# Performance work log

Measured on AMD Instinct MI355X. Metric: run time of the kernel, lower is better.

## Reference

```python
import jax, jax.numpy as jnp
import numpy as np

NEG = -1e9

def _lstm(x, Wih, Whh, b):
    # x: [B,S,D]; PyTorch gate order i,f,g,o; Wih:[4H,D], Whh:[4H,H], b:[4H]
    B = x.shape[0]
    H = Whh.shape[1]
    def step(carry, xt):
        h, c = carry
        g = xt @ Wih.T + h @ Whh.T + b
        i, f, gg, o = jnp.split(g, 4, axis=-1)
        c = jax.nn.sigmoid(f) * c + jax.nn.sigmoid(i) * jnp.tanh(gg)
        h = jax.nn.sigmoid(o) * jnp.tanh(c)
        return (h, c), h
    init = (jnp.zeros((B, H), x.dtype), jnp.zeros((B, H), x.dtype))
    _, hs = jax.lax.scan(step, init, x.transpose(1, 0, 2))
    return hs.transpose(1, 0, 2)  # [B,S,H]

def _bilstm(x, Wih_f, Whh_f, b_f, Wih_b, Whh_b, b_b):
    fwd = _lstm(x, Wih_f, Whh_f, b_f)
    bwd = jnp.flip(_lstm(jnp.flip(x, 1), Wih_b, Whh_b, b_b), 1)
    return jnp.concatenate([fwd, bwd], axis=-1)

def _windowed_attention(h, attn_W, attn_b, window_size):
    # score(i,j) = W @ [h_i, h_j, h_i*h_j] + b, decomposed exactly:
    #   = h_i@w1 + h_j@w2 + (h_i*w3)@h_j + b, masked to |i-j| <= window
    S = h.shape[1]
    w1, w2, w3 = jnp.split(attn_W[0], 3)
    s1 = h @ w1                                   # [B,S]
    s2 = h @ w2                                   # [B,S]
    cross = jnp.einsum('bid,bjd->bij', h * w3, h)  # [B,S,S]
    scores = s1[:, :, None] + s2[:, None, :] + cross + attn_b[0]
    idx = jnp.arange(S)
    band = jnp.abs(idx[:, None] - idx[None, :]) <= window_size
    scores = jnp.where(band, scores, NEG)
    p = jax.nn.softmax(scores, axis=-1)
    return jnp.einsum('bij,bjd->bid', p, h)       # [B,S,H]

def _forward(x, lstm1_Wih_f, lstm1_Whh_f, lstm1_b_f, lstm1_Wih_b, lstm1_Whh_b, lstm1_b_b,
             fc1_W, fc1_b, attn_W, attn_b,
             lstm2_Wih_f, lstm2_Whh_f, lstm2_b_f, lstm2_Wih_b, lstm2_Whh_b, lstm2_b_b,
             l2_W1, l2_b1, l2_W2, l2_b2, l2_W3, l2_b3, window_size):
    # dropout layers are identity at inference
    lstm_out = _bilstm(x, lstm1_Wih_f, lstm1_Whh_f, lstm1_b_f,
                       lstm1_Wih_b, lstm1_Whh_b, lstm1_b_b)          # [B,S,768]
    h = lstm_out @ fc1_W.T + fc1_b                                    # [B,S,384]
    attn = _windowed_attention(h, attn_W, attn_b, window_size)        # [B,S,384]
    h_cat = jnp.concatenate([h, attn], axis=-1)                       # [B,S,768]
    lstm_out2 = _bilstm(h_cat, lstm2_Wih_f, lstm2_Whh_f, lstm2_b_f,
                        lstm2_Wih_b, lstm2_Whh_b, lstm2_b_b)          # [B,S,768]
    h2 = lstm_out2 @ fc1_W.T + fc1_b                                  # fc1 reused, as in source
    y = jax.nn.relu(h2 @ l2_W1.T + l2_b1)
    y = jax.nn.relu(y @ l2_W2.T + l2_b2)
    return y @ l2_W3.T + l2_b3                                        # [B,S,1]

def setup_inputs() -> dict:
    key = jax.random.key(0)
    ks = iter(jax.random.split(key, 32))
    D, H, B, S = 768, 384, 16, 1024
    sc = 0.02
    def rn(shape):
        return jax.random.normal(next(ks), shape, dtype=jnp.float32) * sc
    inp = {'x': jax.random.normal(next(ks), (B, S, D), dtype=jnp.float32)}
    for name in ('lstm1', 'lstm2'):
        inp[f'{name}_Wih_f'] = rn((4 * H, D)); inp[f'{name}_Whh_f'] = rn((4 * H, H))
        inp[f'{name}_b_f'] = rn((4 * H,))
        inp[f'{name}_Wih_b'] = rn((4 * H, D)); inp[f'{name}_Whh_b'] = rn((4 * H, H))
        inp[f'{name}_b_b'] = rn((4 * H,))
    inp['fc1_W'] = rn((H, D)); inp['fc1_b'] = rn((H,))
    inp['attn_W'] = rn((1, 3 * H)); inp['attn_b'] = rn((1,))
    inp['l2_W1'] = rn((256, H)); inp['l2_b1'] = rn((256,))
    inp['l2_W2'] = rn((96, 256)); inp['l2_b2'] = rn((96,))
    inp['l2_W3'] = rn((1, 96)); inp['l2_b3'] = rn((1,))
    inp['window_size'] = 32
    return inp

def reference(x, lstm1_Wih_f, lstm1_Whh_f, lstm1_b_f, lstm1_Wih_b, lstm1_Whh_b, lstm1_b_b,
              fc1_W, fc1_b, attn_W, attn_b,
              lstm2_Wih_f, lstm2_Whh_f, lstm2_b_f, lstm2_Wih_b, lstm2_Whh_b, lstm2_b_b,
              l2_W1, l2_b1, l2_W2, l2_b2, l2_W3, l2_b3, window_size):
    return _forward(x, lstm1_Wih_f, lstm1_Whh_f, lstm1_b_f, lstm1_Wih_b, lstm1_Whh_b, lstm1_b_b,
                    fc1_W, fc1_b, attn_W, attn_b,
                    lstm2_Wih_f, lstm2_Whh_f, lstm2_b_f, lstm2_Wih_b, lstm2_Whh_b, lstm2_b_b,
                    l2_W1, l2_b1, l2_W2, l2_b2, l2_W3, l2_b3, window_size)
```

## Files before the change

kernel.cpp:

```cpp
#include <hip/hip_runtime.h>
#include <hip/hip_bf16.h>
#include <hip/hip_fp16.h>
#include <type_traits>

#define S_LEN 1024
#define BATCH 16
#define HID   384
#define DIN   768

#define GRP 8
#define UPB 48
#define NTHR 384

__device__ __forceinline__ float sigf(float x)     { return 1.f/(1.f + __expf(-x)); }
__device__ __forceinline__ float tanhfast(float x) { return 1.f - 2.f/(__expf(2.f*x) + 1.f); }

__device__ __forceinline__ __half2 unpackh2(float f) {
    return __builtin_bit_cast(__half2, f);
}

typedef __attribute__((ext_vector_type(8))) _Float16 f16x8;
typedef __attribute__((ext_vector_type(4))) float f32x4;

__global__ void zero_kernel(unsigned long long* hx)
{
    int i = blockIdx.x * blockDim.x + threadIdx.x;
    if (i < 32*2*HID) hx[i] = 0ull;
}

__global__ void prep16(const float* __restrict__ wf, const float* __restrict__ wb,
                       __half* __restrict__ o)
{
    int i = blockIdx.x * 256 + threadIdx.x;
    if (i < 147456) {
        const float4 a = ((const float4*)wf)[i];
        const float4 b = ((const float4*)wb)[i];
        __half2* of = (__half2*)o;
        of[2*i]   = __halves2half2(__float2half(a.x), __float2half(a.y));
        of[2*i+1] = __halves2half2(__float2half(a.z), __float2half(a.w));
        __half2* ob = (__half2*)(o + 589824);
        ob[2*i]   = __halves2half2(__float2half(b.x), __float2half(b.y));
        ob[2*i+1] = __halves2half2(__float2half(b.z), __float2half(b.w));
    }
}

__global__ __launch_bounds__(256) void prep_wc(
    const float* __restrict__ fc1W,
    const float* __restrict__ fc1b,
    const float* __restrict__ w1,
    const float* __restrict__ b1,
    float* __restrict__ Wc,
    float* __restrict__ bc)
{
    __shared__ float wr[384];
    const int n = blockIdx.x;
    const int tid = threadIdx.x;
    if (tid < 192) {
        const float2 v = *(const float2*)(w1 + (size_t)n * 384 + tid * 2);
        wr[tid*2] = v.x; wr[tid*2+1] = v.y;
    }
    __syncthreads();
    float s0 = 0.f, s1 = 0.f, s2 = 0.f;
    for (int j = 0; j < 384; j++) {
        const float w = wr[j];
        const float* fr = fc1W + (size_t)j * 768;
        s0 += w * fr[tid]; s1 += w * fr[tid + 256]; s2 += w * fr[tid + 512];
    }
    Wc[(size_t)n*768 + tid]       = s0;
    Wc[(size_t)n*768 + tid + 256] = s1;
    Wc[(size_t)n*768 + tid + 512] = s2;
    if (tid == 0) {
        float s = b1[n];
        for (int j = 0; j < 384; j++) s += wr[j] * fc1b[j];
        bc[n] = s;
    }
}

template<int RELU, typename OT>
__global__ __launch_bounds__(256) void gemm_f16(
    const float* __restrict__ A, int ldA,
    const float* __restrict__ W,
    const float* __restrict__ bias,
    OT* __restrict__ C, int ldC,
    int K)
{
    __shared__ char Al[128 * 128];
    __shared__ char Bl[128 * 128];
    const int tid  = threadIdx.x;
    const int m0   = blockIdx.x * 128;
    const int n0   = blockIdx.y * 128;
    const int wid  = tid >> 6, lane = tid & 63;
    const int wm   = (wid >> 1) * 64, wn = (wid & 1) * 64;
    const int fr   = lane & 15, fq = lane >> 4;

    f32x4 acc[4][4] = {};

    const int srow = tid >> 1;
    const int sseg = (tid & 1) * 32;

    for (int k0 = 0; k0 < K; k0 += 64) {
        {
            const float* ap = A + (size_t)(m0 + srow) * ldA + k0 + sseg;
            const float* wp = W + (size_t)(n0 + srow) * K   + k0 + sseg;
            _Float16 ta[32], tw[32];
            #pragma unroll
            for (int q = 0; q < 8; q++) {
                const float4 va = *(const float4*)(ap + q * 4);
                const float4 vw = *(const float4*)(wp + q * 4);
                ta[4*q+0] = (_Float16)va.x; ta[4*q+1] = (_Float16)va.y;
                ta[4*q+2] = (_Float16)va.z; ta[4*q+3] = (_Float16)va.w;
                tw[4*q+0] = (_Float16)vw.x; tw[4*q+1] = (_Float16)vw.y;
                tw[4*q+2] = (_Float16)vw.z; tw[4*q+3] = (_Float16)vw.w;
            }
            const int xr = (srow & 7) << 4;
            #pragma unroll
            for (int c = 0; c < 4; c++) {
                const int col = (sseg * 2 + c * 16) ^ xr;
                *(f16x8*)(Al + srow * 128 + col) = *(f16x8*)&ta[c * 8];
                *(f16x8*)(Bl + srow * 128 + col) = *(f16x8*)&tw[c * 8];
            }
        }
        __syncthreads();

        #pragma unroll
        for (int kc = 0; kc < 2; kc++) {
            f16x8 af[4], bf[4];
            #pragma unroll
            for (int mt = 0; mt < 4; mt++) {
                const int r = wm + mt * 16 + fr;
                af[mt] = *(const f16x8*)(Al + r * 128 + ((kc * 64 + fq * 16) ^ ((r & 7) << 4)));
            }
            #pragma unroll
            for (int nt = 0; nt < 4; nt++) {
                const int r = wn + nt * 16 + fr;
                bf[nt] = *(const f16x8*)(Bl + r * 128 + ((kc * 64 + fq * 16) ^ ((r & 7) << 4)));
            }
            #pragma unroll
            for (int mt = 0; mt < 4; mt++)
                #pragma unroll
                for (int nt = 0; nt < 4; nt++)
                    acc[mt][nt] = __builtin_amdgcn_mfma_f32_16x16x32_f16(
                        af[mt], bf[nt], acc[mt][nt], 0, 0, 0);
        }
        __syncthreads();
    }

    #pragma unroll
    for (int mt = 0; mt < 4; mt++) {
        #pragma unroll
        for (int nt = 0; nt < 4; nt++) {
            const int n = n0 + wn + nt * 16 + fr;
            const float bv = bias[n];
            #pragma unroll
            for (int j = 0; j < 4; j++) {
                const int m = m0 + wm + mt * 16 + fq * 4 + j;
                float v = acc[mt][nt][j] + bv;
                if (RELU) v = fmaxf(v, 0.f);
                if constexpr (std::is_same_v<OT, __hip_bfloat16>)
                    C[(size_t)m * ldC + n] = __float2bfloat16(v);
                else
                    C[(size_t)m * ldC + n] = v;
            }
        }
    }
}

template<int RELU, typename OT>
__global__ __launch_bounds__(256) void gemm_nt(
    const float* __restrict__ A, int ldA,
    const float* __restrict__ W,
    const float* __restrict__ bias,
    OT* __restrict__ C, int ldC,
    int M, int N, int K)
{
    __shared__ float As[16][132];
    __shared__ float Ws[16][68];
    const int tid = threadIdx.x;
    const int m0 = blockIdx.x * 128;
    const int n0 = blockIdx.y * 64;
    const int tm = (tid & 15) * 8;
    const int tn = (tid >> 4) * 4;

    float acc[8][4];
    #pragma unroll
    for (int i = 0; i < 8; i++)
        #pragma unroll
        for (int j = 0; j < 4; j++) acc[i][j] = 0.f;

    const int lrow = tid >> 2;
    const int lk   = (tid & 3) * 4;

    for (int k0 = 0; k0 < K; k0 += 16) {
        #pragma unroll
        for (int p = 0; p < 2; p++) {
            const int r = lrow + p * 64;
            const float4 av = *(const float4*)(A + (size_t)(m0 + r) * ldA + k0 + lk);
            As[lk+0][r] = av.x; As[lk+1][r] = av.y; As[lk+2][r] = av.z; As[lk+3][r] = av.w;
        }
        {
            float4 wv = make_float4(0.f, 0.f, 0.f, 0.f);
            if (n0 + lrow < N) wv = *(const float4*)(W + (size_t)(n0 + lrow) * K + k0 + lk);
            Ws[lk+0][lrow] = wv.x; Ws[lk+1][lrow] = wv.y; Ws[lk+2][lrow] = wv.z; Ws[lk+3][lrow] = wv.w;
        }
        __syncthreads();
        #pragma unroll
        for (int k = 0; k < 16; k++) {
            const float4 a0 = *(const float4*)&As[k][tm];
            const float4 a1 = *(const float4*)&As[k][tm + 4];
            const float4 bv = *(const float4*)&Ws[k][tn];
            const float am[8] = {a0.x, a0.y, a0.z, a0.w, a1.x, a1.y, a1.z, a1.w};
            const float bb[4] = {bv.x, bv.y, bv.z, bv.w};
            #pragma unroll
            for (int i = 0; i < 8; i++)
                #pragma unroll
                for (int j = 0; j < 4; j++) acc[i][j] += am[i] * bb[j];
        }
        __syncthreads();
    }

    #pragma unroll
    for (int i = 0; i < 8; i++) {
        const int m = m0 + tm + i;
        #pragma unroll
        for (int j = 0; j < 4; j++) {
            const int n = n0 + tn + j;
            if (n < N) {
                float v = acc[i][j] + bias[n];
                if (RELU) v = fmaxf(v, 0.f);
                if constexpr (std::is_same_v<OT, __hip_bfloat16>)
                    C[(size_t)m * ldC + n] = __float2bfloat16(v);
                else
                    C[(size_t)m * ldC + n] = v;
            }
        }
    }
}

__global__ __launch_bounds__(NTHR) void lstm_scan(
    const __hip_bfloat16* __restrict__ gatesF, const __hip_bfloat16* __restrict__ gatesB,
    const __half* __restrict__ wh16,
    float* __restrict__ out, unsigned long long* hx_all, int epoch)
{
    __shared__ float hl[2][HID];

    const int blk = blockIdx.x;
    const int g   = blk & 31;
    const int m   = blk >> 5;
    const int dir = g >> 4;
    const int b   = g & 15;
    const int u0  = m * UPB;

    const __hip_bfloat16* gates = dir ? gatesB : gatesF;
    const __half* wh = wh16 + (size_t)dir * 589824;
    unsigned long long* hx = hx_all + g * (2 * HID);

    const int tid = threadIdx.x;
    const int rr  = tid >> 3;
    const int ss  = tid & 7;
    const int ug  = u0 + rr;
    const bool owner = (ss == 0);

    float c_state = 0.f;
    const unsigned tbase = (unsigned)epoch * 2048u;

    for (int t = 0; t < S_LEN; t++) {
        const int tt = dir ? (S_LEN - 1 - t) : t;

        float gx0 = 0.f, gx1 = 0.f, gx2 = 0.f, gx3 = 0.f;
        if (owner) {
            const __hip_bfloat16* gp = gates + ((size_t)(b * S_LEN + tt)) * (4 * HID) + ug;
            gx0 = __bfloat162float(gp[0]);
            gx1 = __bfloat162float(gp[HID]);
            gx2 = __bfloat162float(gp[2 * HID]);
            gx3 = __bfloat162float(gp[3 * HID]);
        }

        if (t == 0) {
            if (tid < 128) {
                hl[0][tid] = 0.f; hl[0][tid + 128] = 0.f; hl[0][tid + 256] = 0.f;
            }
        } else if (tid < 128) {
            const unsigned long long* src = hx + ((t + 1) & 1) * HID;
            float* dst = hl[t & 1];
            const unsigned tgt = tbase + (unsigned)t;
            int pend = 7;
            long guard = 0;
            do {
                if (pend & 1) {
                    const unsigned long long q = __hip_atomic_load(src + tid,
                        __ATOMIC_RELAXED, __HIP_MEMORY_SCOPE_AGENT);
                    if ((unsigned)(q >> 32) >= tgt) {
                        dst[tid] = __uint_as_float((unsigned)q); pend &= ~1;
                    }
                }
                if (pend & 2) {
                    const unsigned long long q = __hip_atomic_load(src + tid + 128,
                        __ATOMIC_RELAXED, __HIP_MEMORY_SCOPE_AGENT);
                    if ((unsigned)(q >> 32) >= tgt) {
                        dst[tid + 128] = __uint_as_float((unsigned)q); pend &= ~2;
                    }
                }
                if (pend & 4) {
                    const unsigned long long q = __hip_atomic_load(src + tid + 256,
                        __ATOMIC_RELAXED, __HIP_MEMORY_SCOPE_AGENT);
                    if ((unsigned)(q >> 32) >= tgt) {
                        dst[tid + 256] = __uint_as_float((unsigned)q); pend &= ~4;
                    }
                }
                if (!pend) break;
                __builtin_amdgcn_s_sleep(1);
            } while (++guard < (1L << 22));
        }
        __syncthreads();

        const float* hsl = hl[t & 1];
        float a0 = 0.f, a1 = 0.f, a2 = 0.f, a3 = 0.f;
        #pragma unroll
        for (int jj = 0; jj < 6; jj++) {
            const float4 h40 = *(const float4*)(hsl + ss * 8 + 64 * jj);
            const float4 h41 = *(const float4*)(hsl + ss * 8 + 64 * jj + 4);
            #pragma unroll
            for (int gt = 0; gt < 4; gt++) {
                const float4 wv = *(const float4*)(wh + ((size_t)(gt * HID + ug)) * HID + ss * 8 + 64 * jj);
                const __half2 p0 = unpackh2(wv.x), p1 = unpackh2(wv.y),
                              p2 = unpackh2(wv.z), p3 = unpackh2(wv.w);
                float s = __low2float(p0) * h40.x + __high2float(p0) * h40.y
                        + __low2float(p1) * h40.z + __high2float(p1) * h40.w
                        + __low2float(p2) * h41.x + __high2float(p2) * h41.y
                        + __low2float(p3) * h41.z + __high2float(p3) * h41.w;
                if (gt == 0) a0 += s;
                else if (gt == 1) a1 += s;
                else if (gt == 2) a2 += s;
                else a3 += s;
            }
        }
        a0 += __shfl_xor(a0, 1, 64); a0 += __shfl_xor(a0, 2, 64); a0 += __shfl_xor(a0, 4, 64);
        a1 += __shfl_xor(a1, 1, 64); a1 += __shfl_xor(a1, 2, 64); a1 += __shfl_xor(a1, 4, 64);
        a2 += __shfl_xor(a2, 1, 64); a2 += __shfl_xor(a2, 2, 64); a2 += __shfl_xor(a2, 4, 64);
        a3 += __shfl_xor(a3, 1, 64); a3 += __shfl_xor(a3, 2, 64); a3 += __shfl_xor(a3, 4, 64);

        if (owner) {
            const float ii = sigf(a0 + gx0);
            const float ff = sigf(a1 + gx1);
            const float gg = tanhfast(a2 + gx2);
            const float oo = sigf(a3 + gx3);
            c_state = ff * c_state + ii * gg;
            const float hn = oo * tanhfast(c_state);
            const unsigned long long pk =
                ((unsigned long long)(tbase + (unsigned)t + 1u) << 32) |
                (unsigned long long)__float_as_uint(hn);
            __hip_atomic_store(hx + (t & 1) * HID + ug, pk,
                               __ATOMIC_RELAXED, __HIP_MEMORY_SCOPE_AGENT);
            out[((size_t)(b * S_LEN + tt)) * (2 * HID) + dir * HID + ug] = hn;
        }
    }
}

__global__ __launch_bounds__(256) void attn_win(
    const float* __restrict__ hcat,
    const float* __restrict__ attnW,
    float* __restrict__ ocat,
    const int* __restrict__ wsz_p)
{
    __shared__ float q[HID];
    __shared__ float sc[96];
    __shared__ float p[96];
    const int blk = blockIdx.x;
    const int b = blk >> 10, i = blk & 1023;
    const int W = *wsz_p;
    const int jlo = max(i - W, 0), jhi = min(i + W, S_LEN - 1);
    const int nj = jhi - jlo + 1;
    const int tid = threadIdx.x;
    const float* hrow = hcat + (size_t)b * S_LEN * 768;

    if (tid < 96) {
        const float4 hv = *(const float4*)(hrow + (size_t)i * 768 + tid * 4);
        const float4 w3 = *(const float4*)(attnW + 768 + tid * 4);
        const float4 w2 = *(const float4*)(attnW + 384 + tid * 4);
        float4 r;
        r.x = hv.x*w3.x + w2.x; r.y = hv.y*w3.y + w2.y;
        r.z = hv.z*w3.z + w2.z; r.w = hv.w*w3.w + w2.w;
        *(float4*)(q + tid * 4) = r;
    }
    __syncthreads();

    const int wv = tid >> 6, lane = tid & 63;
    for (int jj = wv; jj < nj; jj += 4) {
        const float* hj = hrow + (size_t)(jlo + jj) * 768;
        float s = 0.f;
        #pragma unroll
        for (int c = 0; c < 6; c++) { const int d = lane + 64*c; s += q[d] * hj[d]; }
        #pragma unroll
        for (int st = 1; st < 64; st <<= 1) s += __shfl_xor(s, st, 64);
        if (lane == 0) sc[jj] = s;
    }
    __syncthreads();

    if (tid < 64) {
        float v1 = (tid < nj) ? sc[tid] : -3e38f;
        float v2 = (64 + tid < nj) ? sc[64 + tid] : -3e38f;
        float m = fmaxf(v1, v2);
        #pragma unroll
        for (int st = 1; st < 64; st <<= 1) m = fmaxf(m, __shfl_xor(m, st, 64));
        float e1 = (tid < nj) ? __expf(v1 - m) : 0.f;
        float e2 = (64 + tid < nj) ? __expf(v2 - m) : 0.f;
        float sum = e1 + e2;
        #pragma unroll
        for (int st = 1; st < 64; st <<= 1) sum += __shfl_xor(sum, st, 64);
        const float inv = 1.f / sum;
        if (tid < nj) p[tid] = e1 * inv;
        if (64 + tid < nj) p[64 + tid] = e2 * inv;
    }
    __syncthreads();

    if (tid < 192) {
        const int d = tid * 2;
        float s0 = 0.f, s1 = 0.f;
        for (int jj = 0; jj < nj; jj++) {
            const float* hj = hrow + (size_t)(jlo + jj) * 768 + d;
            const float pj = p[jj];
            s0 += pj * hj[0]; s1 += pj * hj[1];
        }
        float* o = ocat + (size_t)b * S_LEN * 768 + (size_t)i * 768 + 384 + d;
        o[0] = s0; o[1] = s1;
    }
}

__global__ __launch_bounds__(256) void final_dot(
    const float* __restrict__ y2, const float* __restrict__ W3,
    const float* __restrict__ b3, float* __restrict__ outp)
{
    __shared__ float w[96];
    const int tid = threadIdx.x;
    if (tid < 96) w[tid] = W3[tid];
    __syncthreads();
    const int r = blockIdx.x * 256 + tid;
    const float* row = y2 + (size_t)r * 96;
    float s = 0.f;
    #pragma unroll
    for (int c = 0; c < 24; c++) {
        const float4 v = ((const float4*)row)[c];
        s += v.x*w[c*4] + v.y*w[c*4+1] + v.z*w[c*4+2] + v.w*w[c*4+3];
    }
    outp[r] = s + b3[0];
}

extern "C" void kernel_launch(void* const* d_in, const int* in_sizes, int n_in,
                              void* d_out, int out_size, void* d_ws, size_t ws_size,
                              hipStream_t stream)
{
    const float* x        = (const float*)d_in[0];
    const float* l1_Wih_f = (const float*)d_in[1];
    const float* l1_Whh_f = (const float*)d_in[2];
    const float* l1_b_f   = (const float*)d_in[3];
    const float* l1_Wih_b = (const float*)d_in[4];
    const float* l1_Whh_b = (const float*)d_in[5];
    const float* l1_b_b   = (const float*)d_in[6];
    const float* l2_Wih_f = (const float*)d_in[7];
    const float* l2_Whh_f = (const float*)d_in[8];
    const float* l2_b_f   = (const float*)d_in[9];
    const float* l2_Wih_b = (const float*)d_in[10];
    const float* l2_Whh_b = (const float*)d_in[11];
    const float* l2_b_b   = (const float*)d_in[12];
    const float* fc1_W    = (const float*)d_in[13];
    const float* fc1_b    = (const float*)d_in[14];
    const float* attn_W   = (const float*)d_in[15];
    const float* w1       = (const float*)d_in[17];
    const float* b1       = (const float*)d_in[18];
    const float* w2       = (const float*)d_in[19];
    const float* b2       = (const float*)d_in[20];
    const float* w3       = (const float*)d_in[21];
    const float* b3       = (const float*)d_in[22];
    const int*   wsz      = (const int*)d_in[23];

    char* wsb = (char*)d_ws;
    __hip_bfloat16*     gF  = (__hip_bfloat16*)(wsb);
    __hip_bfloat16*     gB  = (__hip_bfloat16*)(wsb +  50331648);
    float*              seq = (float*)(wsb + 100663296);
    float*              hct = (float*)(wsb + 150994944);
    unsigned long long* hx  = (unsigned long long*)(wsb + 201326592);
    __half*             w16 = (__half*)hct;
    float*              Wc  = (float*)(wsb);
    float*              bc  = (float*)(wsb + 786432);
    float*              y1  = (float*)(wsb +  50331648);
    float*              y2  = (float*)(wsb +  50331648 + 16777216);

    const int M = BATCH * S_LEN;
    dim3 tb(256);

    zero_kernel<<<dim3(96), tb, 0, stream>>>(hx);
    prep16<<<dim3(576), tb, 0, stream>>>(l1_Whh_f, l1_Whh_b, w16);
    gemm_f16<0, __hip_bfloat16><<<dim3(M/128, 12), tb, 0, stream>>>(x, DIN, l1_Wih_f, l1_b_f, gF, 1536, DIN);
    gemm_f16<0, __hip_bfloat16><<<dim3(M/128, 12), tb, 0, stream>>>(x, DIN, l1_Wih_b, l1_b_b, gB, 1536, DIN);
    lstm_scan<<<dim3(256), dim3(NTHR), 0, stream>>>(gF, gB, w16, seq, hx, 0);

    gemm_f16<0, float><<<dim3(M/128, 3), tb, 0, stream>>>(seq, 768, fc1_W, fc1_b, hct, 768, 768);
    attn_win<<<dim3(M), tb, 0, stream>>>(hct, attn_W, hct, wsz);

    gemm_f16<0, __hip_bfloat16><<<dim3(M/128, 12), tb, 0, stream>>>(hct, 768, l2_Wih_f, l2_b_f, gF, 1536, 768);
    gemm_f16<0, __hip_bfloat16><<<dim3(M/128, 12), tb, 0, stream>>>(hct, 768, l2_Wih_b, l2_b_b, gB, 1536, 768);
    prep16<<<dim3(576), tb, 0, stream>>>(l2_Whh_f, l2_Whh_b, w16);
    lstm_scan<<<dim3(256), dim3(NTHR), 0, stream>>>(gF, gB, w16, seq, hx, 1);

    prep_wc<<<dim3(256), tb, 0, stream>>>(fc1_W, fc1_b, w1, b1, Wc, bc);
    gemm_f16<1, float><<<dim3(M/128, 2), tb, 0, stream>>>(seq, 768, Wc, bc, y1, 256, 768);
    gemm_nt<1, float><<<dim3(M/128, 2), tb, 0, stream>>>(y1, 256, w2, b2, y2, 96, M, 96, 256);
    final_dot<<<dim3(M/256), tb, 0, stream>>>(y2, w3, b3, (float*)d_out);
}
```

Measured before the change: 5.879 ms.

## Add tiled fp16 windowed attention kernel sharing a key slab per 64 queries

Adds an attention kernel that handles 64 query rows per block. It stages the union of their key windows in shared memory as fp16 and computes scores with packed fdot2 instructions, then does softmax and the weighted sum from the shared copy. The per-row kernel is still launched but exits early when the window is at most 32, so the tiled path runs at the default window size. This cuts redundant global reads of neighbouring rows, at the cost of fp16 precision in the score and output math and a large shared-memory footprint that limits occupancy.

```diff
diff --git a/kernel.cpp b/kernel.cpp
--- a/kernel.cpp
+++ b/kernel.cpp
@@ -20,7 +20,23 @@
 }
 
 typedef __attribute__((ext_vector_type(8))) _Float16 f16x8;
+typedef __attribute__((ext_vector_type(2))) _Float16 f16x2;
 typedef __attribute__((ext_vector_type(4))) float f32x4;
+
+__device__ __forceinline__ float dot8(f16x8 a, f16x8 b, float c) {
+#if __has_builtin(__builtin_amdgcn_fdot2)
+    union { f16x8 v; f16x2 h[4]; } ua, ub;
+    ua.v = a; ub.v = b;
+    #pragma unroll
+    for (int e = 0; e < 4; e++)
+        c = __builtin_amdgcn_fdot2(ua.h[e], ub.h[e], c, false);
+    return c;
+#else
+    #pragma unroll
+    for (int e = 0; e < 8; e++) c += (float)a[e] * (float)b[e];
+    return c;
+#endif
+}
 
 __global__ void zero_kernel(unsigned long long* hx)
 {
@@ -356,6 +372,129 @@
     }
 }
 
+__global__ __launch_bounds__(256) void attn_tile(
+    const float* __restrict__ hcat,
+    const float* __restrict__ attnW,
+    float* __restrict__ ocat,
+    const int* __restrict__ wsz_p)
+{
+    const int W = *wsz_p;
+    if (W > 32) return;
+
+    __shared__ __half hs[128 * 392];
+    __shared__ __half qsc[4][384];
+    __shared__ __half w3h[384];
+    __shared__ __half w2h[384];
+    __shared__ float  sc[64 * 68];
+
+    const int blk = blockIdx.x;
+    const int b   = blk >> 4;
+    const int i0  = (blk & 15) * 64;
+    const int tid = threadIdx.x;
+    const int wv  = tid >> 6, lane = tid & 63;
+    const int jlo0 = max(i0 - W, 0);
+    const int jhi  = min(i0 + 63 + W, S_LEN - 1);
+    const int nr   = jhi - jlo0 + 1;
+    const int nj   = 2 * W + 1;
+    const float* hrow = hcat + (size_t)b * S_LEN * 768;
+
+    if (tid < 192) {
+        const float2 a = *(const float2*)(attnW + 768 + tid * 2);
+        const float2 c = *(const float2*)(attnW + 384 + tid * 2);
+        ((__half2*)w3h)[tid] = __halves2half2(__float2half(a.x), __float2half(a.y));
+        ((__half2*)w2h)[tid] = __halves2half2(__float2half(c.x), __float2half(c.y));
+    }
+    {
+        const int r  = tid >> 1;
+        const int h0 = (tid & 1) * 192;
+        if (r < nr) {
+            const float* src = hrow + (size_t)(jlo0 + r) * 768 + h0;
+            __half* dst = hs + r * 392 + h0;
+            #pragma unroll
+            for (int c = 0; c < 24; c++) {
+                const float4 v0 = *(const float4*)(src + c * 8);
+                const float4 v1 = *(const float4*)(src + c * 8 + 4);
+                f16x8 pk;
+                pk[0] = (_Float16)v0.x; pk[1] = (_Float16)v0.y;
+                pk[2] = (_Float16)v0.z; pk[3] = (_Float16)v0.w;
+                pk[4] = (_Float16)v1.x; pk[5] = (_Float16)v1.y;
+                pk[6] = (_Float16)v1.z; pk[7] = (_Float16)v1.w;
+                *(f16x8*)(dst + c * 8) = pk;
+            }
+        }
+    }
+    __syncthreads();
+
+    for (int k = 0; k < 16; k++) {
+        const int i  = wv * 16 + k;
+        const int qi = i0 + i;
+        const int ir = qi - jlo0;
+        if (lane < 48) {
+            const f16x8 hi8 = *(const f16x8*)(hs + ir * 392 + lane * 8);
+            const f16x8 w38 = *(const f16x8*)(w3h + lane * 8);
+            const f16x8 w28 = *(const f16x8*)(w2h + lane * 8);
+            f16x8 q8;
+            #pragma unroll
+            for (int e = 0; e < 8; e++) q8[e] = hi8[e] * w38[e] + w28[e];
+            *(f16x8*)(&qsc[wv][lane * 8]) = q8;
+        }
+        asm volatile("s_waitcnt lgkmcnt(0)" ::: "memory");
+        __builtin_amdgcn_sched_barrier(0);
+        for (int jj = lane; jj < nj; jj += 64) {
+            const int j = qi - W + jj;
+            float s = -3e38f;
+            if (j >= 0 && j < S_LEN) {
+                const int jr = j - jlo0;
+                float acc = 0.f;
+                #pragma unroll
+                for (int c = 0; c < 48; c++) {
+                    const f16x8 q8  = *(const f16x8*)(&qsc[wv][c * 8]);
+                    const f16x8 hj8 = *(const f16x8*)(hs + jr * 392 + c * 8);
+                    acc = dot8(q8, hj8, acc);
+                }
+                s = acc;
+            }
+            sc[i * 68 + jj] = s;
+        }
+    }
+    __syncthreads();
+
+    if (tid < 64) {
+        const int i = tid;
+        float mx = -3e38f;
+        for (int jj = 0; jj < nj; jj++) mx = fmaxf(mx, sc[i * 68 + jj]);
+        float sum = 0.f;
+        for (int jj = 0; jj < nj; jj++) {
+            const float e = __expf(sc[i * 68 + jj] - mx);
+            sc[i * 68 + jj] = e; sum += e;
+        }
+        const float inv = 1.f / sum;
+        for (int jj = 0; jj < nj; jj++) sc[i * 68 + jj] *= inv;
+    }
+    __syncthreads();
+
+    for (int k = 0; k < 16; k++) {
+        const int i  = wv * 16 + k;
+        const int qi = i0 + i;
+        if (lane < 48) {
+            float o[8] = {0.f, 0.f, 0.f, 0.f, 0.f, 0.f, 0.f, 0.f};
+            for (int jj = 0; jj < nj; jj++) {
+                const int j = qi - W + jj;
+                if (j < 0 || j >= S_LEN) continue;
+                const float p = sc[i * 68 + jj];
+                const f16x8 hj8 = *(const f16x8*)(hs + (j - jlo0) * 392 + lane * 8);
+                #pragma unroll
+                for (int e = 0; e < 8; e++) o[e] += p * (float)hj8[e];
+            }
+            float* op = ocat + (size_t)b * S_LEN * 768 + (size_t)qi * 768 + 384 + lane * 8;
+            float4 o0 = {o[0], o[1], o[2], o[3]};
+            float4 o1 = {o[4], o[5], o[6], o[7]};
+            *(float4*)op = o0;
+            *(float4*)(op + 4) = o1;
+        }
+    }
+}
+
 __global__ __launch_bounds__(256) void attn_win(
     const float* __restrict__ hcat,
     const float* __restrict__ attnW,
@@ -365,9 +504,10 @@
     __shared__ float q[HID];
     __shared__ float sc[96];
     __shared__ float p[96];
+    const int W = *wsz_p;
+    if (W <= 32) return;
     const int blk = blockIdx.x;
     const int b = blk >> 10, i = blk & 1023;
-    const int W = *wsz_p;
     const int jlo = max(i - W, 0), jhi = min(i + W, S_LEN - 1);
     const int nj = jhi - jlo + 1;
     const int tid = threadIdx.x;
@@ -495,6 +635,7 @@
     lstm_scan<<<dim3(256), dim3(NTHR), 0, stream>>>(gF, gB, w16, seq, hx, 0);
 
     gemm_f16<0, float><<<dim3(M/128, 3), tb, 0, stream>>>(seq, 768, fc1_W, fc1_b, hct, 768, 768);
+    attn_tile<<<dim3(256), tb, 0, stream>>>(hct, attn_W, hct, wsz);
     attn_win<<<dim3(M), tb, 0, stream>>>(hct, attn_W, hct, wsz);
 
     gemm_f16<0, __hip_bfloat16><<<dim3(M/128, 12), tb, 0, stream>>>(hct, 768, l2_Wih_f, l2_b_f, gF, 1536, 768);
```

New measurement: 5.961 ms. About the same (+1.4%).
